# Optimization experiments

Hardware: AMD Instinct MI355X
Metric: run time of the kernel (lower is better)

## Reference

```python
import jax, jax.numpy as jnp
import numpy as np

B, T, C, H = 2, 2048, 1024, 16
D = C // H  # head_dim = 64


def setup_inputs() -> dict:
    key = jax.random.key(0)
    k1, k2, k3 = jax.random.split(key, 3)
    scale = 0.02
    return {
        "x": jax.random.normal(k1, (B, T, C), dtype=jnp.float32),
        "w_qkv": jax.random.normal(k2, (C, 3 * C), dtype=jnp.float32) * scale,
        "b_qkv": jnp.zeros((3 * C,), dtype=jnp.float32),
        "w_out": jax.random.normal(k3, (C, C), dtype=jnp.float32) * scale,
        "b_out": jnp.zeros((C,), dtype=jnp.float32),
    }


def reference(x, w_qkv, b_qkv, w_out, b_out):
    b, t, c = x.shape
    qkv = x @ w_qkv + b_qkv                       # [b, t, 3c]
    q, k, v = jnp.split(qkv, 3, axis=-1)
    # [b, t, c] -> [b, h, t, d]
    q = q.reshape(b, t, H, D).transpose(0, 2, 1, 3)
    k = k.reshape(b, t, H, D).transpose(0, 2, 1, 3)
    v = v.reshape(b, t, H, D).transpose(0, 2, 1, 3)
    scores = jnp.einsum("bhqd,bhkd->bhqk", q, k) / jnp.sqrt(jnp.asarray(D, dtype=q.dtype))
    causal = jnp.tril(jnp.ones((t, t), dtype=bool))
    scores = jnp.where(causal, scores, jnp.finfo(scores.dtype).min)
    attn = jax.nn.softmax(scores, axis=-1)        # [b, h, q, k]
    out = jnp.einsum("bhqk,bhkd->bhqd", attn, v)  # [b, h, t, d]
    out = out.transpose(0, 2, 1, 3).reshape(b, t, c)
    return out @ w_out + b_out
```

## Files before the change

kernel.cpp:

```cpp
#include <hip/hip_runtime.h>

#define B_ 2
#define T_ 2048
#define C_ 1024
#define H_ 16
#define D_ 64

using bf16x8 = __attribute__((ext_vector_type(8))) short;
using f32x4  = __attribute__((ext_vector_type(4))) float;

static __device__ __forceinline__ short f2bf(float f) {
  unsigned u = __builtin_bit_cast(unsigned, f);
  unsigned r = u + 0x7fffu + ((u >> 16) & 1u);
  return (short)(r >> 16);
}

#define GLD16(gp, lp) __builtin_amdgcn_global_load_lds( \
    (const __attribute__((address_space(1))) void*)(gp), \
    (__attribute__((address_space(3))) void*)(lp), 16, 0, 0)

__global__ __launch_bounds__(256) void cast_f32_bf16(const float* __restrict__ in,
                                                     short* __restrict__ out) {
  int i = blockIdx.x * blockDim.x + threadIdx.x;
  float4 v = ((const float4*)in)[i];
  short4 o;
  o.x = f2bf(v.x); o.y = f2bf(v.y); o.z = f2bf(v.z); o.w = f2bf(v.w);
  ((short4*)out)[i] = o;
}

__global__ __launch_bounds__(256) void transpose_cast(const float* __restrict__ in,
                                                      short* __restrict__ out,
                                                      int R, int N) {
  __shared__ float tile[32][33];
  int bx = blockIdx.x * 32, by = blockIdx.y * 32;
  int tx = threadIdx.x, ty = threadIdx.y;
  #pragma unroll
  for (int j = 0; j < 32; j += 8)
    tile[ty + j][tx] = in[(size_t)(by + ty + j) * N + bx + tx];
  __syncthreads();
  #pragma unroll
  for (int j = 0; j < 32; j += 8)
    out[(size_t)(bx + ty + j) * R + by + tx] = f2bf(tile[tx][ty + j]);
}

__global__ __launch_bounds__(256) void gemm_qkv(const short* __restrict__ A,
                                                const short* __restrict__ Bt,
                                                const float* __restrict__ bias,
                                                short* __restrict__ Qo,
                                                short* __restrict__ Ko,
                                                short* __restrict__ Vo) {
  __shared__ short sA[128 * 64];
  __shared__ short sB[128 * 64];
  const int tid = threadIdx.x;
  const int w = tid >> 6, lane = tid & 63;
  const int wm = w >> 1, wn = w & 1;
  const int g = lane >> 4, r16 = lane & 15;
  const int m0 = blockIdx.x * 128, n0 = blockIdx.y * 128;
  const int krow = lane >> 3, kslot = lane & 7;

  f32x4 acc[4][4] = {};

  for (int k0 = 0; k0 < 1024; k0 += 64) {
    __syncthreads();
    #pragma unroll
    for (int p = 0; p < 4; ++p) {
      int rbase = w * 32 + p * 8;
      int row = rbase + krow;
      GLD16(&A[(size_t)(m0 + row) * 1024 + k0 + ((kslot ^ (row & 7)) * 8)], &sA[rbase * 64]);
      GLD16(&Bt[(size_t)(n0 + row) * 1024 + k0 + ((kslot ^ (row & 7)) * 8)], &sB[rbase * 64]);
    }
    __syncthreads();
    bf16x8 af[4][2], bf[4][2];
    #pragma unroll
    for (int mi = 0; mi < 4; ++mi) {
      int row = wm * 64 + mi * 16 + r16;
      #pragma unroll
      for (int c = 0; c < 2; ++c)
        af[mi][c] = *(const bf16x8*)&sA[row * 64 + (((c * 4 + g) ^ (row & 7)) * 8)];
    }
    #pragma unroll
    for (int ni = 0; ni < 4; ++ni) {
      int row = wn * 64 + ni * 16 + r16;
      #pragma unroll
      for (int c = 0; c < 2; ++c)
        bf[ni][c] = *(const bf16x8*)&sB[row * 64 + (((c * 4 + g) ^ (row & 7)) * 8)];
    }
    __builtin_amdgcn_s_setprio(1);
    #pragma unroll
    for (int mi = 0; mi < 4; ++mi)
      #pragma unroll
      for (int ni = 0; ni < 4; ++ni) {
        acc[mi][ni] = __builtin_amdgcn_mfma_f32_16x16x32_bf16(af[mi][0], bf[ni][0], acc[mi][ni], 0, 0, 0);
        acc[mi][ni] = __builtin_amdgcn_mfma_f32_16x16x32_bf16(af[mi][1], bf[ni][1], acc[mi][ni], 0, 0, 0);
      }
    __builtin_amdgcn_s_setprio(0);
  }

  #pragma unroll
  for (int mi = 0; mi < 4; ++mi) {
    #pragma unroll
    for (int ni = 0; ni < 4; ++ni) {
      int n = n0 + wn * 64 + ni * 16 + r16;
      float bv = bias[n];
      int which = n >> 10;
      int c = n & 1023;
      int hh = c >> 6, d = c & 63;
      short* dst = (which == 0) ? Qo : ((which == 1) ? Ko : Vo);
      float sc = (which == 0) ? 0.18033688f : 1.0f;
      #pragma unroll
      for (int rr = 0; rr < 4; ++rr) {
        int m = m0 + wm * 64 + mi * 16 + g * 4 + rr;
        int b = m >> 11, t = m & 2047;
        dst[(size_t)((b * H_ + hh) * T_ + t) * D_ + d] = f2bf((acc[mi][ni][rr] + bv) * sc);
      }
    }
  }
}

__global__ __launch_bounds__(256) void gemm_out(const short* __restrict__ A,
                                                const short* __restrict__ Bt,
                                                const float* __restrict__ bias,
                                                float* __restrict__ Out) {
  __shared__ short sA[128 * 64];
  __shared__ short sB[128 * 64];
  const int tid = threadIdx.x;
  const int w = tid >> 6, lane = tid & 63;
  const int wm = w >> 1, wn = w & 1;
  const int g = lane >> 4, r16 = lane & 15;
  const int m0 = blockIdx.x * 128, n0 = blockIdx.y * 128;
  const int krow = lane >> 3, kslot = lane & 7;

  f32x4 acc[4][4] = {};

  for (int k0 = 0; k0 < 1024; k0 += 64) {
    __syncthreads();
    #pragma unroll
    for (int p = 0; p < 4; ++p) {
      int rbase = w * 32 + p * 8;
      int row = rbase + krow;
      GLD16(&A[(size_t)(m0 + row) * 1024 + k0 + ((kslot ^ (row & 7)) * 8)], &sA[rbase * 64]);
      GLD16(&Bt[(size_t)(n0 + row) * 1024 + k0 + ((kslot ^ (row & 7)) * 8)], &sB[rbase * 64]);
    }
    __syncthreads();
    bf16x8 af[4][2], bf[4][2];
    #pragma unroll
    for (int mi = 0; mi < 4; ++mi) {
      int row = wm * 64 + mi * 16 + r16;
      #pragma unroll
      for (int c = 0; c < 2; ++c)
        af[mi][c] = *(const bf16x8*)&sA[row * 64 + (((c * 4 + g) ^ (row & 7)) * 8)];
    }
    #pragma unroll
    for (int ni = 0; ni < 4; ++ni) {
      int row = wn * 64 + ni * 16 + r16;
      #pragma unroll
      for (int c = 0; c < 2; ++c)
        bf[ni][c] = *(const bf16x8*)&sB[row * 64 + (((c * 4 + g) ^ (row & 7)) * 8)];
    }
    __builtin_amdgcn_s_setprio(1);
    #pragma unroll
    for (int mi = 0; mi < 4; ++mi)
      #pragma unroll
      for (int ni = 0; ni < 4; ++ni) {
        acc[mi][ni] = __builtin_amdgcn_mfma_f32_16x16x32_bf16(af[mi][0], bf[ni][0], acc[mi][ni], 0, 0, 0);
        acc[mi][ni] = __builtin_amdgcn_mfma_f32_16x16x32_bf16(af[mi][1], bf[ni][1], acc[mi][ni], 0, 0, 0);
      }
    __builtin_amdgcn_s_setprio(0);
  }

  #pragma unroll
  for (int mi = 0; mi < 4; ++mi) {
    #pragma unroll
    for (int ni = 0; ni < 4; ++ni) {
      int n = n0 + wn * 64 + ni * 16 + r16;
      float bv = bias[n];
      #pragma unroll
      for (int rr = 0; rr < 4; ++rr) {
        int m = m0 + wm * 64 + mi * 16 + g * 4 + rr;
        Out[(size_t)m * 1024 + n] = acc[mi][ni][rr] + bv;
      }
    }
  }
}

__global__ __launch_bounds__(256, 4) void attn_fwd(const short* __restrict__ Q,
                                                   const short* __restrict__ K,
                                                   const short* __restrict__ V,
                                                   short* __restrict__ O) {
  __shared__ short sK[3][64 * 64];
  __shared__ short vT[2][64 * 64];

  const int tid = threadIdx.x;
  const int w = tid >> 6, lane = tid & 63;
  const int g = lane >> 4, r16 = lane & 15;
  const int bh = blockIdx.x;
  const int b = bh >> 4, hh = bh & 15;
  const int qi = 31 - (int)blockIdx.y;
  const int q0 = qi * 64;

  const short* Qh = Q + (size_t)bh * T_ * D_;
  const short* Kh = K + (size_t)bh * T_ * D_;
  const short* Vh = V + (size_t)bh * T_ * D_;

  const int krow_in_wave = lane >> 3;
  const int kslot = lane & 7;
  const int kp = tid & 31;
  const int vd0 = (tid >> 5) * 8;
  const int vchunk = (kp >> 4) * 4 + ((kp & 7) >> 1);
  const int velem  = ((kp >> 3) & 1) * 4 + 2 * (kp & 1);

  const int qrow_a = q0 + w * 16 + r16;
  bf16x8 qf[2];
  qf[0] = *(const bf16x8*)&Qh[(size_t)qrow_a * 64 + g * 8];
  qf[1] = *(const bf16x8*)&Qh[(size_t)qrow_a * 64 + 32 + g * 8];

  f32x4 o[4] = {};
  float m_ = -1e30f, l_ = 0.f;

  const int nkt = qi + 1;

  {
    int4 v0 = *(const int4*)&Vh[(size_t)(2 * kp) * 64 + vd0];
    int4 v1 = *(const int4*)&Vh[(size_t)(2 * kp + 1) * 64 + vd0];
    #pragma unroll
    for (int p = 0; p < 2; ++p) {
      int row = w * 16 + p * 8 + krow_in_wave;
      GLD16(&Kh[(size_t)row * 64 + ((kslot ^ (row & 7)) * 8)], &sK[0][(w * 16 + p * 8) * 64]);
    }
    if (nkt > 1) {
      #pragma unroll
      for (int p = 0; p < 2; ++p) {
        int row = w * 16 + p * 8 + krow_in_wave;
        GLD16(&Kh[(size_t)(64 + row) * 64 + ((kslot ^ (row & 7)) * 8)],
              &sK[1][(w * 16 + p * 8) * 64]);
      }
    }
    const short* a0 = (const short*)&v0;
    const short* a1 = (const short*)&v1;
    #pragma unroll
    for (int j = 0; j < 8; ++j) {
      int d = vd0 + j;
      int val = ((int)(unsigned short)a0[j]) | (((int)(unsigned short)a1[j]) << 16);
      *(int*)&vT[0][d * 64 + ((vchunk ^ j) * 8) + velem] = val;
    }
    if (nkt > 1) asm volatile("s_waitcnt vmcnt(2)" ::: "memory");
    else         asm volatile("s_waitcnt vmcnt(0)" ::: "memory");
    asm volatile("s_waitcnt lgkmcnt(0)" ::: "memory");
    __builtin_amdgcn_sched_barrier(0);
    __builtin_amdgcn_s_barrier();
    __builtin_amdgcn_sched_barrier(0);
  }

  for (int kt = 0; kt < nkt; ++kt) {
    const int cur3 = kt % 3;
    const int curv = kt & 1;
    const bool pf1 = (kt + 1 < nkt);
    const bool pf2 = (kt + 2 < nkt);

    int4 vn0, vn1;
    if (pf1) {
      const int k1 = (kt + 1) * 64;
      vn0 = *(const int4*)&Vh[(size_t)(k1 + 2 * kp) * 64 + vd0];
      vn1 = *(const int4*)&Vh[(size_t)(k1 + 2 * kp + 1) * 64 + vd0];
    }
    if (pf2) {
      const int k2 = (kt + 2) * 64;
      const int nb = (kt + 2) % 3;
      #pragma unroll
      for (int p = 0; p < 2; ++p) {
        int row = w * 16 + p * 8 + krow_in_wave;
        GLD16(&Kh[(size_t)(k2 + row) * 64 + ((kslot ^ (row & 7)) * 8)],
              &sK[nb][(w * 16 + p * 8) * 64]);
      }
    }
    __builtin_amdgcn_sched_barrier(0);

    f32x4 s[4] = {};
    __builtin_amdgcn_s_setprio(1);
    #pragma unroll
    for (int nt = 0; nt < 4; ++nt) {
      const int row = nt * 16 + r16;
      const int sw8 = r16 & 7;
      bf16x8 kf0 = *(const bf16x8*)&sK[cur3][row * 64 + ((g ^ sw8) * 8)];
      bf16x8 kf1 = *(const bf16x8*)&sK[cur3][row * 64 + (((4 + g) ^ sw8) * 8)];
      s[nt] = __builtin_amdgcn_mfma_f32_16x16x32_bf16(kf0, qf[0], s[nt], 0, 0, 0);
      s[nt] = __builtin_amdgcn_mfma_f32_16x16x32_bf16(kf1, qf[1], s[nt], 0, 0, 0);
    }
    __builtin_amdgcn_s_setprio(0);

    if (kt == nkt - 1) {
      const int qrow = w * 16 + r16;
      #pragma unroll
      for (int nt = 0; nt < 4; ++nt)
        #pragma unroll
        for (int rr = 0; rr < 4; ++rr)
          if (nt * 16 + 4 * g + rr > qrow) s[nt][rr] = -1e30f;
    }
    float pmax = s[0][0];
    #pragma unroll
    for (int nt = 0; nt < 4; ++nt)
      #pragma unroll
      for (int rr = 0; rr < 4; ++rr)
        pmax = fmaxf(pmax, s[nt][rr]);
    pmax = fmaxf(pmax, __shfl_xor(pmax, 16));
    pmax = fmaxf(pmax, __shfl_xor(pmax, 32));
    if (!__all(pmax - m_ <= 8.0f)) {
      float mn = fmaxf(m_, pmax);
      float al = __builtin_amdgcn_exp2f(m_ - mn);
      m_ = mn;
      l_ *= al;
      float av[4];
      #pragma unroll
      for (int rr = 0; rr < 4; ++rr) av[rr] = __shfl(al, 4 * g + rr, 16);
      #pragma unroll
      for (int nt = 0; nt < 4; ++nt)
        #pragma unroll
        for (int rr = 0; rr < 4; ++rr) o[nt][rr] *= av[rr];
    }
    float rs = 0.f;
    #pragma unroll
    for (int nt = 0; nt < 4; ++nt)
      #pragma unroll
      for (int rr = 0; rr < 4; ++rr) {
        float p = __builtin_amdgcn_exp2f(s[nt][rr] - m_);
        s[nt][rr] = p;
        rs += p;
      }
    rs += __shfl_xor(rs, 16);
    rs += __shfl_xor(rs, 32);
    l_ += rs;
    int pk[8];
    #pragma unroll
    for (int nt = 0; nt < 4; ++nt)
      #pragma unroll
      for (int h = 0; h < 2; ++h)
        asm("v_cvt_pk_bf16_f32 %0, %1, %2"
            : "=v"(pk[nt * 2 + h])
            : "v"(s[nt][2 * h]), "v"(s[nt][2 * h + 1]));

    bf16x8 pa[2];
    {
      int4 t0; t0.x = pk[0]; t0.y = pk[1]; t0.z = pk[2]; t0.w = pk[3];
      int4 t1; t1.x = pk[4]; t1.y = pk[5]; t1.z = pk[6]; t1.w = pk[7];
      pa[0] = __builtin_bit_cast(bf16x8, t0);
      pa[1] = __builtin_bit_cast(bf16x8, t1);
    }
    __builtin_amdgcn_s_setprio(1);
    #pragma unroll
    for (int nt = 0; nt < 4; ++nt) {
      const int d = nt * 16 + r16;
      bf16x8 vb0 = *(const bf16x8*)&vT[curv][d * 64 + ((g ^ (d & 7)) * 8)];
      bf16x8 vb1 = *(const bf16x8*)&vT[curv][d * 64 + (((4 + g) ^ (d & 7)) * 8)];
      o[nt] = __builtin_amdgcn_mfma_f32_16x16x32_bf16(pa[0], vb0, o[nt], 0, 0, 0);
      o[nt] = __builtin_amdgcn_mfma_f32_16x16x32_bf16(pa[1], vb1, o[nt], 0, 0, 0);
    }
    __builtin_amdgcn_s_setprio(0);

    if (pf1) {
      const short* a0 = (const short*)&vn0;
      const short* a1 = (const short*)&vn1;
      #pragma unroll
      for (int j = 0; j < 8; ++j) {
        int d = vd0 + j;
        int val = ((int)(unsigned short)a0[j]) | (((int)(unsigned short)a1[j]) << 16);
        *(int*)&vT[curv ^ 1][d * 64 + ((vchunk ^ j) * 8) + velem] = val;
      }
      if (pf2) asm volatile("s_waitcnt vmcnt(2)" ::: "memory");
      else     asm volatile("s_waitcnt vmcnt(0)" ::: "memory");
      asm volatile("s_waitcnt lgkmcnt(0)" ::: "memory");
      __builtin_amdgcn_sched_barrier(0);
      __builtin_amdgcn_s_barrier();
      __builtin_amdgcn_sched_barrier(0);
    }
  }

  float lv[4];
  #pragma unroll
  for (int rr = 0; rr < 4; ++rr) lv[rr] = __shfl(l_, 4 * g + rr, 16);
  #pragma unroll
  for (int nt = 0; nt < 4; ++nt) {
    int d = nt * 16 + r16;
    #pragma unroll
    for (int rr = 0; rr < 4; ++rr) {
      int t = q0 + w * 16 + 4 * g + rr;
      O[(size_t)(b * T_ + t) * C_ + hh * 64 + d] = f2bf(o[nt][rr] / lv[rr]);
    }
  }
}

extern "C" void kernel_launch(void* const* d_in, const int* in_sizes, int n_in,
                              void* d_out, int out_size, void* d_ws, size_t ws_size,
                              hipStream_t stream) {
  const float* x     = (const float*)d_in[0];
  const float* w_qkv = (const float*)d_in[1];
  const float* b_qkv = (const float*)d_in[2];
  const float* w_out = (const float*)d_in[3];
  const float* b_out = (const float*)d_in[4];
  float* out = (float*)d_out;

  char* ws = (char*)d_ws;
  if (ws_size < (size_t)(40u << 20)) return;

  short* xb     = (short*)(ws);
  short* wqkvT  = (short*)(ws + ((size_t)8u << 20));
  short* woutT  = (short*)(ws + ((size_t)14u << 20));
  short* Qb     = (short*)(ws + ((size_t)16u << 20));
  short* Kb     = (short*)(ws + ((size_t)24u << 20));
  short* Vb     = (short*)(ws + ((size_t)32u << 20));
  short* attn_o = xb;

  cast_f32_bf16<<<4096, 256, 0, stream>>>(x, xb);
  transpose_cast<<<dim3(96, 32), dim3(32, 8), 0, stream>>>(w_qkv, wqkvT, 1024, 3072);
  transpose_cast<<<dim3(32, 32), dim3(32, 8), 0, stream>>>(w_out, woutT, 1024, 1024);
  gemm_qkv<<<dim3(32, 24), 256, 0, stream>>>(xb, wqkvT, b_qkv, Qb, Kb, Vb);
  attn_fwd<<<dim3(32, 32), 256, 0, stream>>>(Qb, Kb, Vb, attn_o);
  gemm_out<<<dim3(32, 8), 256, 0, stream>>>(attn_o, woutT, b_out, out);
}
```

Baseline: 125.1 us.

## Write V transposed and permuted from QKV GEMM; attention reads K/V directly to registers

The QKV GEMM epilogue now stores V as a per-head D x T layout with a permuted token order, so the attention kernel can load V fragments straight from global memory in MFMA operand order. The attention kernel drops all LDS staging, barriers and the in-kernel V transpose. Each block now has 2 waves and each wave owns 32 query rows (two 16-row groups), which reuses each K/V fragment twice. Removing LDS and synchronisation costs redundant global loads per wave, since K and V are no longer shared across waves, and the transposed V store in the GEMM epilogue is strided.

```diff
diff --git a/kernel.cpp b/kernel.cpp
--- a/kernel.cpp
+++ b/kernel.cpp
@@ -105,13 +105,19 @@
       int which = n >> 10;
       int c = n & 1023;
       int hh = c >> 6, d = c & 63;
-      short* dst = (which == 0) ? Qo : ((which == 1) ? Ko : Vo);
       float sc = (which == 0) ? 0.18033688f : 1.0f;
       #pragma unroll
       for (int rr = 0; rr < 4; ++rr) {
         int m = m0 + wm * 64 + mi * 16 + g * 4 + rr;
         int b = m >> 11, t = m & 2047;
-        dst[(size_t)((b * H_ + hh) * T_ + t) * D_ + d] = f2bf((acc[mi][ni][rr] + bv) * sc);
+        short val = f2bf((acc[mi][ni][rr] + bv) * sc);
+        if (which == 2) {
+          int tp = (t & ~0x1C) | ((t & 0xC) << 1) | ((t & 0x10) >> 2);
+          Vo[(size_t)((b * H_ + hh) * D_ + d) * T_ + tp] = val;
+        } else {
+          short* dst = (which == 0) ? Qo : Ko;
+          dst[(size_t)((b * H_ + hh) * T_ + t) * D_ + d] = val;
+        }
       }
     }
   }
@@ -183,207 +189,157 @@
   }
 }
 
-__global__ __launch_bounds__(256, 4) void attn_fwd(const short* __restrict__ Q,
+__global__ __launch_bounds__(128, 2) void attn_fwd(const short* __restrict__ Q,
                                                    const short* __restrict__ K,
-                                                   const short* __restrict__ V,
+                                                   const short* __restrict__ Vt,
                                                    short* __restrict__ O) {
-  __shared__ short sK[3][64 * 64];
-  __shared__ short vT[2][64 * 64];
-
   const int tid = threadIdx.x;
   const int w = tid >> 6, lane = tid & 63;
   const int g = lane >> 4, r16 = lane & 15;
   const int bh = blockIdx.x;
   const int b = bh >> 4, hh = bh & 15;
-  const int qi = 31 - (int)blockIdx.y;
-  const int q0 = qi * 64;
+  const int qt = 31 - (int)blockIdx.y;
+  const int qs = qt * 64 + w * 32;
 
   const short* Qh = Q + (size_t)bh * T_ * D_;
   const short* Kh = K + (size_t)bh * T_ * D_;
-  const short* Vh = V + (size_t)bh * T_ * D_;
-
-  const int krow_in_wave = lane >> 3;
-  const int kslot = lane & 7;
-  const int kp = tid & 31;
-  const int vd0 = (tid >> 5) * 8;
-  const int vchunk = (kp >> 4) * 4 + ((kp & 7) >> 1);
-  const int velem  = ((kp >> 3) & 1) * 4 + 2 * (kp & 1);
-
-  const int qrow_a = q0 + w * 16 + r16;
-  bf16x8 qf[2];
-  qf[0] = *(const bf16x8*)&Qh[(size_t)qrow_a * 64 + g * 8];
-  qf[1] = *(const bf16x8*)&Qh[(size_t)qrow_a * 64 + 32 + g * 8];
-
-  f32x4 o[4] = {};
-  float m_ = -1e30f, l_ = 0.f;
-
-  const int nkt = qi + 1;
-
-  {
-    int4 v0 = *(const int4*)&Vh[(size_t)(2 * kp) * 64 + vd0];
-    int4 v1 = *(const int4*)&Vh[(size_t)(2 * kp + 1) * 64 + vd0];
-    #pragma unroll
-    for (int p = 0; p < 2; ++p) {
-      int row = w * 16 + p * 8 + krow_in_wave;
-      GLD16(&Kh[(size_t)row * 64 + ((kslot ^ (row & 7)) * 8)], &sK[0][(w * 16 + p * 8) * 64]);
-    }
-    if (nkt > 1) {
-      #pragma unroll
-      for (int p = 0; p < 2; ++p) {
-        int row = w * 16 + p * 8 + krow_in_wave;
-        GLD16(&Kh[(size_t)(64 + row) * 64 + ((kslot ^ (row & 7)) * 8)],
-              &sK[1][(w * 16 + p * 8) * 64]);
-      }
-    }
-    const short* a0 = (const short*)&v0;
-    const short* a1 = (const short*)&v1;
-    #pragma unroll
-    for (int j = 0; j < 8; ++j) {
-      int d = vd0 + j;
-      int val = ((int)(unsigned short)a0[j]) | (((int)(unsigned short)a1[j]) << 16);
-      *(int*)&vT[0][d * 64 + ((vchunk ^ j) * 8) + velem] = val;
-    }
-    if (nkt > 1) asm volatile("s_waitcnt vmcnt(2)" ::: "memory");
-    else         asm volatile("s_waitcnt vmcnt(0)" ::: "memory");
-    asm volatile("s_waitcnt lgkmcnt(0)" ::: "memory");
-    __builtin_amdgcn_sched_barrier(0);
-    __builtin_amdgcn_s_barrier();
-    __builtin_amdgcn_sched_barrier(0);
+  const short* Vh = Vt + (size_t)bh * D_ * T_;
+
+  bf16x8 qf[2][2];
+  #pragma unroll
+  for (int u = 0; u < 2; ++u) {
+    const size_t qoff = (size_t)(qs + u * 16 + r16) * 64;
+    qf[u][0] = *(const bf16x8*)&Qh[qoff + g * 8];
+    qf[u][1] = *(const bf16x8*)&Qh[qoff + 32 + g * 8];
+  }
+
+  f32x4 o[2][4] = {};
+  float m_[2] = {-1e30f, -1e30f}, l_[2] = {0.f, 0.f};
+
+  const int nkt = qs / 64 + 1;
+
+  bf16x8 kf[4][2];
+  #pragma unroll
+  for (int nt = 0; nt < 4; ++nt) {
+    const size_t koff = (size_t)(nt * 16 + r16) * 64;
+    kf[nt][0] = *(const bf16x8*)&Kh[koff + g * 8];
+    kf[nt][1] = *(const bf16x8*)&Kh[koff + 32 + g * 8];
   }
 
   for (int kt = 0; kt < nkt; ++kt) {
-    const int cur3 = kt % 3;
-    const int curv = kt & 1;
-    const bool pf1 = (kt + 1 < nkt);
-    const bool pf2 = (kt + 2 < nkt);
-
-    int4 vn0, vn1;
-    if (pf1) {
-      const int k1 = (kt + 1) * 64;
-      vn0 = *(const int4*)&Vh[(size_t)(k1 + 2 * kp) * 64 + vd0];
-      vn1 = *(const int4*)&Vh[(size_t)(k1 + 2 * kp + 1) * 64 + vd0];
-    }
-    if (pf2) {
-      const int k2 = (kt + 2) * 64;
-      const int nb = (kt + 2) % 3;
-      #pragma unroll
-      for (int p = 0; p < 2; ++p) {
-        int row = w * 16 + p * 8 + krow_in_wave;
-        GLD16(&Kh[(size_t)(k2 + row) * 64 + ((kslot ^ (row & 7)) * 8)],
-              &sK[nb][(w * 16 + p * 8) * 64]);
-      }
-    }
-    __builtin_amdgcn_sched_barrier(0);
-
-    f32x4 s[4] = {};
+    const int k0 = kt * 64;
+
+    bf16x8 vb[4][2];
+    #pragma unroll
+    for (int nt = 0; nt < 4; ++nt) {
+      const size_t voff = (size_t)(nt * 16 + r16) * T_ + k0;
+      vb[nt][0] = *(const bf16x8*)&Vh[voff + g * 8];
+      vb[nt][1] = *(const bf16x8*)&Vh[voff + 32 + g * 8];
+    }
+
+    f32x4 s[2][4] = {};
     __builtin_amdgcn_s_setprio(1);
     #pragma unroll
     for (int nt = 0; nt < 4; ++nt) {
-      const int row = nt * 16 + r16;
-      const int sw8 = r16 & 7;
-      bf16x8 kf0 = *(const bf16x8*)&sK[cur3][row * 64 + ((g ^ sw8) * 8)];
-      bf16x8 kf1 = *(const bf16x8*)&sK[cur3][row * 64 + (((4 + g) ^ sw8) * 8)];
-      s[nt] = __builtin_amdgcn_mfma_f32_16x16x32_bf16(kf0, qf[0], s[nt], 0, 0, 0);
-      s[nt] = __builtin_amdgcn_mfma_f32_16x16x32_bf16(kf1, qf[1], s[nt], 0, 0, 0);
+      s[0][nt] = __builtin_amdgcn_mfma_f32_16x16x32_bf16(kf[nt][0], qf[0][0], s[0][nt], 0, 0, 0);
+      s[0][nt] = __builtin_amdgcn_mfma_f32_16x16x32_bf16(kf[nt][1], qf[0][1], s[0][nt], 0, 0, 0);
+      s[1][nt] = __builtin_amdgcn_mfma_f32_16x16x32_bf16(kf[nt][0], qf[1][0], s[1][nt], 0, 0, 0);
+      s[1][nt] = __builtin_amdgcn_mfma_f32_16x16x32_bf16(kf[nt][1], qf[1][1], s[1][nt], 0, 0, 0);
     }
     __builtin_amdgcn_s_setprio(0);
 
-    if (kt == nkt - 1) {
-      const int qrow = w * 16 + r16;
+    if (kt + 1 < nkt) {
+      const int k1 = k0 + 64;
+      #pragma unroll
+      for (int nt = 0; nt < 4; ++nt) {
+        const size_t koff = (size_t)(k1 + nt * 16 + r16) * 64;
+        kf[nt][0] = *(const bf16x8*)&Kh[koff + g * 8];
+        kf[nt][1] = *(const bf16x8*)&Kh[koff + 32 + g * 8];
+      }
+    }
+
+    bf16x8 pa[2][2];
+    #pragma unroll
+    for (int u = 0; u < 2; ++u) {
+      if (kt == nkt - 1) {
+        const int qrow = qs + u * 16 + r16;
+        #pragma unroll
+        for (int nt = 0; nt < 4; ++nt)
+          #pragma unroll
+          for (int rr = 0; rr < 4; ++rr)
+            if (k0 + nt * 16 + 4 * g + rr > qrow) s[u][nt][rr] = -1e30f;
+      }
+      float pmax = s[u][0][0];
       #pragma unroll
       for (int nt = 0; nt < 4; ++nt)
         #pragma unroll
         for (int rr = 0; rr < 4; ++rr)
-          if (nt * 16 + 4 * g + rr > qrow) s[nt][rr] = -1e30f;
-    }
-    float pmax = s[0][0];
-    #pragma unroll
-    for (int nt = 0; nt < 4; ++nt)
-      #pragma unroll
-      for (int rr = 0; rr < 4; ++rr)
-        pmax = fmaxf(pmax, s[nt][rr]);
-    pmax = fmaxf(pmax, __shfl_xor(pmax, 16));
-    pmax = fmaxf(pmax, __shfl_xor(pmax, 32));
-    if (!__all(pmax - m_ <= 8.0f)) {
-      float mn = fmaxf(m_, pmax);
-      float al = __builtin_amdgcn_exp2f(m_ - mn);
-      m_ = mn;
-      l_ *= al;
-      float av[4];
-      #pragma unroll
-      for (int rr = 0; rr < 4; ++rr) av[rr] = __shfl(al, 4 * g + rr, 16);
+          pmax = fmaxf(pmax, s[u][nt][rr]);
+      pmax = fmaxf(pmax, __shfl_xor(pmax, 16));
+      pmax = fmaxf(pmax, __shfl_xor(pmax, 32));
+      if (!__all(pmax - m_[u] <= 8.0f)) {
+        float mn = fmaxf(m_[u], pmax);
+        float al = __builtin_amdgcn_exp2f(m_[u] - mn);
+        m_[u] = mn;
+        l_[u] *= al;
+        float av[4];
+        #pragma unroll
+        for (int rr = 0; rr < 4; ++rr) av[rr] = __shfl(al, 4 * g + rr, 16);
+        #pragma unroll
+        for (int nt = 0; nt < 4; ++nt)
+          #pragma unroll
+          for (int rr = 0; rr < 4; ++rr) o[u][nt][rr] *= av[rr];
+      }
+      float rs = 0.f;
       #pragma unroll
       for (int nt = 0; nt < 4; ++nt)
         #pragma unroll
-        for (int rr = 0; rr < 4; ++rr) o[nt][rr] *= av[rr];
-    }
-    float rs = 0.f;
-    #pragma unroll
-    for (int nt = 0; nt < 4; ++nt)
-      #pragma unroll
-      for (int rr = 0; rr < 4; ++rr) {
-        float p = __builtin_amdgcn_exp2f(s[nt][rr] - m_);
-        s[nt][rr] = p;
-        rs += p;
-      }
-    rs += __shfl_xor(rs, 16);
-    rs += __shfl_xor(rs, 32);
-    l_ += rs;
-    int pk[8];
-    #pragma unroll
-    for (int nt = 0; nt < 4; ++nt)
-      #pragma unroll
-      for (int h = 0; h < 2; ++h)
-        asm("v_cvt_pk_bf16_f32 %0, %1, %2"
-            : "=v"(pk[nt * 2 + h])
-            : "v"(s[nt][2 * h]), "v"(s[nt][2 * h + 1]));
-
-    bf16x8 pa[2];
-    {
+        for (int rr = 0; rr < 4; ++rr) {
+          float p = __builtin_amdgcn_exp2f(s[u][nt][rr] - m_[u]);
+          s[u][nt][rr] = p;
+          rs += p;
+        }
+      rs += __shfl_xor(rs, 16);
+      rs += __shfl_xor(rs, 32);
+      l_[u] += rs;
+      int pk[8];
+      #pragma unroll
+      for (int nt = 0; nt < 4; ++nt)
+        #pragma unroll
+        for (int h = 0; h < 2; ++h)
+          asm("v_cvt_pk_bf16_f32 %0, %1, %2"
+              : "=v"(pk[nt * 2 + h])
+              : "v"(s[u][nt][2 * h]), "v"(s[u][nt][2 * h + 1]));
       int4 t0; t0.x = pk[0]; t0.y = pk[1]; t0.z = pk[2]; t0.w = pk[3];
       int4 t1; t1.x = pk[4]; t1.y = pk[5]; t1.z = pk[6]; t1.w = pk[7];
-      pa[0] = __builtin_bit_cast(bf16x8, t0);
-      pa[1] = __builtin_bit_cast(bf16x8, t1);
-    }
+      pa[u][0] = __builtin_bit_cast(bf16x8, t0);
+      pa[u][1] = __builtin_bit_cast(bf16x8, t1);
+    }
+
     __builtin_amdgcn_s_setprio(1);
     #pragma unroll
     for (int nt = 0; nt < 4; ++nt) {
-      const int d = nt * 16 + r16;
-      bf16x8 vb0 = *(const bf16x8*)&vT[curv][d * 64 + ((g ^ (d & 7)) * 8)];
-      bf16x8 vb1 = *(const bf16x8*)&vT[curv][d * 64 + (((4 + g) ^ (d & 7)) * 8)];
-      o[nt] = __builtin_amdgcn_mfma_f32_16x16x32_bf16(pa[0], vb0, o[nt], 0, 0, 0);
-      o[nt] = __builtin_amdgcn_mfma_f32_16x16x32_bf16(pa[1], vb1, o[nt], 0, 0, 0);
+      o[0][nt] = __builtin_amdgcn_mfma_f32_16x16x32_bf16(pa[0][0], vb[nt][0], o[0][nt], 0, 0, 0);
+      o[0][nt] = __builtin_amdgcn_mfma_f32_16x16x32_bf16(pa[0][1], vb[nt][1], o[0][nt], 0, 0, 0);
+      o[1][nt] = __builtin_amdgcn_mfma_f32_16x16x32_bf16(pa[1][0], vb[nt][0], o[1][nt], 0, 0, 0);
+      o[1][nt] = __builtin_amdgcn_mfma_f32_16x16x32_bf16(pa[1][1], vb[nt][1], o[1][nt], 0, 0, 0);
     }
     __builtin_amdgcn_s_setprio(0);
-
-    if (pf1) {
-      const short* a0 = (const short*)&vn0;
-      const short* a1 = (const short*)&vn1;
-      #pragma unroll
-      for (int j = 0; j < 8; ++j) {
-        int d = vd0 + j;
-        int val = ((int)(unsigned short)a0[j]) | (((int)(unsigned short)a1[j]) << 16);
-        *(int*)&vT[curv ^ 1][d * 64 + ((vchunk ^ j) * 8) + velem] = val;
-      }
-      if (pf2) asm volatile("s_waitcnt vmcnt(2)" ::: "memory");
-      else     asm volatile("s_waitcnt vmcnt(0)" ::: "memory");
-      asm volatile("s_waitcnt lgkmcnt(0)" ::: "memory");
-      __builtin_amdgcn_sched_barrier(0);
-      __builtin_amdgcn_s_barrier();
-      __builtin_amdgcn_sched_barrier(0);
-    }
-  }
-
-  float lv[4];
-  #pragma unroll
-  for (int rr = 0; rr < 4; ++rr) lv[rr] = __shfl(l_, 4 * g + rr, 16);
-  #pragma unroll
-  for (int nt = 0; nt < 4; ++nt) {
-    int d = nt * 16 + r16;
-    #pragma unroll
-    for (int rr = 0; rr < 4; ++rr) {
-      int t = q0 + w * 16 + 4 * g + rr;
-      O[(size_t)(b * T_ + t) * C_ + hh * 64 + d] = f2bf(o[nt][rr] / lv[rr]);
+  }
+
+  #pragma unroll
+  for (int u = 0; u < 2; ++u) {
+    float lv[4];
+    #pragma unroll
+    for (int rr = 0; rr < 4; ++rr) lv[rr] = __shfl(l_[u], 4 * g + rr, 16);
+    #pragma unroll
+    for (int nt = 0; nt < 4; ++nt) {
+      int d = nt * 16 + r16;
+      #pragma unroll
+      for (int rr = 0; rr < 4; ++rr) {
+        int t = qs + u * 16 + 4 * g + rr;
+        O[(size_t)(b * T_ + t) * C_ + hh * 64 + d] = f2bf(o[u][nt][rr] / lv[rr]);
+      }
     }
   }
 }
@@ -406,13 +362,13 @@
   short* woutT  = (short*)(ws + ((size_t)14u << 20));
   short* Qb     = (short*)(ws + ((size_t)16u << 20));
   short* Kb     = (short*)(ws + ((size_t)24u << 20));
-  short* Vb     = (short*)(ws + ((size_t)32u << 20));
+  short* Vtb    = (short*)(ws + ((size_t)32u << 20));
   short* attn_o = xb;
 
   cast_f32_bf16<<<4096, 256, 0, stream>>>(x, xb);
   transpose_cast<<<dim3(96, 32), dim3(32, 8), 0, stream>>>(w_qkv, wqkvT, 1024, 3072);
   transpose_cast<<<dim3(32, 32), dim3(32, 8), 0, stream>>>(w_out, woutT, 1024, 1024);
-  gemm_qkv<<<dim3(32, 24), 256, 0, stream>>>(xb, wqkvT, b_qkv, Qb, Kb, Vb);
-  attn_fwd<<<dim3(32, 32), 256, 0, stream>>>(Qb, Kb, Vb, attn_o);
+  gemm_qkv<<<dim3(32, 24), 256, 0, stream>>>(xb, wqkvT, b_qkv, Qb, Kb, Vtb);
+  attn_fwd<<<dim3(32, 32), 128, 0, stream>>>(Qb, Kb, Vtb, attn_o);
   gemm_out<<<dim3(32, 8), 256, 0, stream>>>(attn_o, woutT, b_out, out);
 }
```

New measurement: 156.1 us. 24.8% more time.

## Write V transposed from QKV GEMM and load V fragments directly in attention

Applied to the files above, without the earlier changes.

The QKV GEMM epilogue now stages V tiles through shared memory and writes V in [head, d, t] layout. The attention kernel then loads V MFMA operands straight from global memory into registers, so it no longer transposes V into LDS each tile. K prefetch drops from triple to double buffering, and the hand-tuned waitcnt/barrier sequence becomes a plain __syncthreads per iteration. This removes LDS transpose work and LDS footprint, but V loads now hit global/L2 on the critical path without prefetch, and the extra sync may reduce overlap.

```diff
diff --git a/kernel.cpp b/kernel.cpp
--- a/kernel.cpp
+++ b/kernel.cpp
@@ -48,9 +48,10 @@
                                                 const float* __restrict__ bias,
                                                 short* __restrict__ Qo,
                                                 short* __restrict__ Ko,
-                                                short* __restrict__ Vo) {
-  __shared__ short sA[128 * 64];
-  __shared__ short sB[128 * 64];
+                                                short* __restrict__ Vt) {
+  __shared__ short smem[128 * 132];
+  short* sA = smem;
+  short* sB = smem + 128 * 64;
   const int tid = threadIdx.x;
   const int w = tid >> 6, lane = tid & 63;
   const int wm = w >> 1, wn = w & 1;
@@ -96,23 +97,52 @@
     __builtin_amdgcn_s_setprio(0);
   }
 
-  #pragma unroll
-  for (int mi = 0; mi < 4; ++mi) {
-    #pragma unroll
-    for (int ni = 0; ni < 4; ++ni) {
-      int n = n0 + wn * 64 + ni * 16 + r16;
-      float bv = bias[n];
-      int which = n >> 10;
-      int c = n & 1023;
-      int hh = c >> 6, d = c & 63;
-      short* dst = (which == 0) ? Qo : ((which == 1) ? Ko : Vo);
-      float sc = (which == 0) ? 0.18033688f : 1.0f;
-      #pragma unroll
-      for (int rr = 0; rr < 4; ++rr) {
-        int m = m0 + wm * 64 + mi * 16 + g * 4 + rr;
-        int b = m >> 11, t = m & 2047;
-        dst[(size_t)((b * H_ + hh) * T_ + t) * D_ + d] = f2bf((acc[mi][ni][rr] + bv) * sc);
-      }
+  if (n0 < 2048) {
+    const int which = n0 >> 10;
+    short* dst = (which == 0) ? Qo : Ko;
+    const float sc = (which == 0) ? 0.18033688f : 1.0f;
+    #pragma unroll
+    for (int mi = 0; mi < 4; ++mi) {
+      #pragma unroll
+      for (int ni = 0; ni < 4; ++ni) {
+        int n = n0 + wn * 64 + ni * 16 + r16;
+        float bv = bias[n];
+        int c = n & 1023;
+        int hh = c >> 6, d = c & 63;
+        #pragma unroll
+        for (int rr = 0; rr < 4; ++rr) {
+          int m = m0 + wm * 64 + mi * 16 + g * 4 + rr;
+          int b = m >> 11, t = m & 2047;
+          dst[(size_t)((b * H_ + hh) * T_ + t) * D_ + d] = f2bf((acc[mi][ni][rr] + bv) * sc);
+        }
+      }
+    }
+  } else {
+    __syncthreads();
+    #pragma unroll
+    for (int mi = 0; mi < 4; ++mi) {
+      #pragma unroll
+      for (int ni = 0; ni < 4; ++ni) {
+        int nn = wn * 64 + ni * 16 + r16;
+        float bv = bias[n0 + nn];
+        #pragma unroll
+        for (int rr = 0; rr < 4; ++rr) {
+          int tm = wm * 64 + mi * 16 + g * 4 + rr;
+          smem[tm * 132 + nn] = f2bf(acc[mi][ni][rr] + bv);
+        }
+      }
+    }
+    __syncthreads();
+    const int tinv = (lane & ~0x1C) | ((lane & 0x18) >> 1) | ((lane & 4) << 2);
+    const int b2 = m0 >> 11, t0l = m0 & 2047;
+    const int head0 = b2 * H_ + ((n0 - 2048) >> 6);
+    #pragma unroll 8
+    for (int i = 0; i < 64; ++i) {
+      int half = i >> 5, nnl = i & 31;
+      int nn = w * 32 + nnl;
+      int d = nn & 63, hh2 = nn >> 6;
+      short val = smem[(half * 64 + tinv) * 132 + nn];
+      Vt[((size_t)(head0 + hh2) * D_ + d) * T_ + t0l + half * 64 + lane] = val;
     }
   }
 }
@@ -185,10 +215,9 @@
 
 __global__ __launch_bounds__(256, 4) void attn_fwd(const short* __restrict__ Q,
                                                    const short* __restrict__ K,
-                                                   const short* __restrict__ V,
+                                                   const short* __restrict__ Vt,
                                                    short* __restrict__ O) {
-  __shared__ short sK[3][64 * 64];
-  __shared__ short vT[2][64 * 64];
+  __shared__ short sK[2][64 * 64];
 
   const int tid = threadIdx.x;
   const int w = tid >> 6, lane = tid & 63;
@@ -200,14 +229,10 @@
 
   const short* Qh = Q + (size_t)bh * T_ * D_;
   const short* Kh = K + (size_t)bh * T_ * D_;
-  const short* Vh = V + (size_t)bh * T_ * D_;
+  const short* Vh = Vt + (size_t)bh * D_ * T_;
 
   const int krow_in_wave = lane >> 3;
   const int kslot = lane & 7;
-  const int kp = tid & 31;
-  const int vd0 = (tid >> 5) * 8;
-  const int vchunk = (kp >> 4) * 4 + ((kp & 7) >> 1);
-  const int velem  = ((kp >> 3) & 1) * 4 + 2 * (kp & 1);
 
   const int qrow_a = q0 + w * 16 + r16;
   bf16x8 qf[2];
@@ -219,61 +244,33 @@
 
   const int nkt = qi + 1;
 
-  {
-    int4 v0 = *(const int4*)&Vh[(size_t)(2 * kp) * 64 + vd0];
-    int4 v1 = *(const int4*)&Vh[(size_t)(2 * kp + 1) * 64 + vd0];
-    #pragma unroll
-    for (int p = 0; p < 2; ++p) {
-      int row = w * 16 + p * 8 + krow_in_wave;
-      GLD16(&Kh[(size_t)row * 64 + ((kslot ^ (row & 7)) * 8)], &sK[0][(w * 16 + p * 8) * 64]);
-    }
-    if (nkt > 1) {
+  #pragma unroll
+  for (int p = 0; p < 2; ++p) {
+    int row = w * 16 + p * 8 + krow_in_wave;
+    GLD16(&Kh[(size_t)row * 64 + ((kslot ^ (row & 7)) * 8)], &sK[0][(w * 16 + p * 8) * 64]);
+  }
+  __syncthreads();
+
+  for (int kt = 0; kt < nkt; ++kt) {
+    const int cur = kt & 1;
+    const int k0 = kt * 64;
+
+    bf16x8 vb[4][2];
+    #pragma unroll
+    for (int nt = 0; nt < 4; ++nt) {
+      const size_t voff = (size_t)(nt * 16 + r16) * T_ + k0;
+      vb[nt][0] = *(const bf16x8*)&Vh[voff + g * 8];
+      vb[nt][1] = *(const bf16x8*)&Vh[voff + 32 + g * 8];
+    }
+    if (kt + 1 < nkt) {
+      const int k1 = k0 + 64;
       #pragma unroll
       for (int p = 0; p < 2; ++p) {
         int row = w * 16 + p * 8 + krow_in_wave;
-        GLD16(&Kh[(size_t)(64 + row) * 64 + ((kslot ^ (row & 7)) * 8)],
-              &sK[1][(w * 16 + p * 8) * 64]);
-      }
-    }
-    const short* a0 = (const short*)&v0;
-    const short* a1 = (const short*)&v1;
-    #pragma unroll
-    for (int j = 0; j < 8; ++j) {
-      int d = vd0 + j;
-      int val = ((int)(unsigned short)a0[j]) | (((int)(unsigned short)a1[j]) << 16);
-      *(int*)&vT[0][d * 64 + ((vchunk ^ j) * 8) + velem] = val;
-    }
-    if (nkt > 1) asm volatile("s_waitcnt vmcnt(2)" ::: "memory");
-    else         asm volatile("s_waitcnt vmcnt(0)" ::: "memory");
-    asm volatile("s_waitcnt lgkmcnt(0)" ::: "memory");
-    __builtin_amdgcn_sched_barrier(0);
-    __builtin_amdgcn_s_barrier();
-    __builtin_amdgcn_sched_barrier(0);
-  }
-
-  for (int kt = 0; kt < nkt; ++kt) {
-    const int cur3 = kt % 3;
-    const int curv = kt & 1;
-    const bool pf1 = (kt + 1 < nkt);
-    const bool pf2 = (kt + 2 < nkt);
-
-    int4 vn0, vn1;
-    if (pf1) {
-      const int k1 = (kt + 1) * 64;
-      vn0 = *(const int4*)&Vh[(size_t)(k1 + 2 * kp) * 64 + vd0];
-      vn1 = *(const int4*)&Vh[(size_t)(k1 + 2 * kp + 1) * 64 + vd0];
-    }
-    if (pf2) {
-      const int k2 = (kt + 2) * 64;
-      const int nb = (kt + 2) % 3;
-      #pragma unroll
-      for (int p = 0; p < 2; ++p) {
-        int row = w * 16 + p * 8 + krow_in_wave;
-        GLD16(&Kh[(size_t)(k2 + row) * 64 + ((kslot ^ (row & 7)) * 8)],
-              &sK[nb][(w * 16 + p * 8) * 64]);
-      }
-    }
-    __builtin_amdgcn_sched_barrier(0);
+        GLD16(&Kh[(size_t)(k1 + row) * 64 + ((kslot ^ (row & 7)) * 8)],
+              &sK[cur ^ 1][(w * 16 + p * 8) * 64]);
+      }
+    }
 
     f32x4 s[4] = {};
     __builtin_amdgcn_s_setprio(1);
@@ -281,8 +278,8 @@
     for (int nt = 0; nt < 4; ++nt) {
       const int row = nt * 16 + r16;
       const int sw8 = r16 & 7;
-      bf16x8 kf0 = *(const bf16x8*)&sK[cur3][row * 64 + ((g ^ sw8) * 8)];
-      bf16x8 kf1 = *(const bf16x8*)&sK[cur3][row * 64 + (((4 + g) ^ sw8) * 8)];
+      bf16x8 kf0 = *(const bf16x8*)&sK[cur][row * 64 + ((g ^ sw8) * 8)];
+      bf16x8 kf1 = *(const bf16x8*)&sK[cur][row * 64 + (((4 + g) ^ sw8) * 8)];
       s[nt] = __builtin_amdgcn_mfma_f32_16x16x32_bf16(kf0, qf[0], s[nt], 0, 0, 0);
       s[nt] = __builtin_amdgcn_mfma_f32_16x16x32_bf16(kf1, qf[1], s[nt], 0, 0, 0);
     }
@@ -348,30 +345,12 @@
     __builtin_amdgcn_s_setprio(1);
     #pragma unroll
     for (int nt = 0; nt < 4; ++nt) {
-      const int d = nt * 16 + r16;
-      bf16x8 vb0 = *(const bf16x8*)&vT[curv][d * 64 + ((g ^ (d & 7)) * 8)];
-      bf16x8 vb1 = *(const bf16x8*)&vT[curv][d * 64 + (((4 + g) ^ (d & 7)) * 8)];
-      o[nt] = __builtin_amdgcn_mfma_f32_16x16x32_bf16(pa[0], vb0, o[nt], 0, 0, 0);
-      o[nt] = __builtin_amdgcn_mfma_f32_16x16x32_bf16(pa[1], vb1, o[nt], 0, 0, 0);
+      o[nt] = __builtin_amdgcn_mfma_f32_16x16x32_bf16(pa[0], vb[nt][0], o[nt], 0, 0, 0);
+      o[nt] = __builtin_amdgcn_mfma_f32_16x16x32_bf16(pa[1], vb[nt][1], o[nt], 0, 0, 0);
     }
     __builtin_amdgcn_s_setprio(0);
 
-    if (pf1) {
-      const short* a0 = (const short*)&vn0;
-      const short* a1 = (const short*)&vn1;
-      #pragma unroll
-      for (int j = 0; j < 8; ++j) {
-        int d = vd0 + j;
-        int val = ((int)(unsigned short)a0[j]) | (((int)(unsigned short)a1[j]) << 16);
-        *(int*)&vT[curv ^ 1][d * 64 + ((vchunk ^ j) * 8) + velem] = val;
-      }
-      if (pf2) asm volatile("s_waitcnt vmcnt(2)" ::: "memory");
-      else     asm volatile("s_waitcnt vmcnt(0)" ::: "memory");
-      asm volatile("s_waitcnt lgkmcnt(0)" ::: "memory");
-      __builtin_amdgcn_sched_barrier(0);
-      __builtin_amdgcn_s_barrier();
-      __builtin_amdgcn_sched_barrier(0);
-    }
+    __syncthreads();
   }
 
   float lv[4];
@@ -406,13 +385,13 @@
   short* woutT  = (short*)(ws + ((size_t)14u << 20));
   short* Qb     = (short*)(ws + ((size_t)16u << 20));
   short* Kb     = (short*)(ws + ((size_t)24u << 20));
-  short* Vb     = (short*)(ws + ((size_t)32u << 20));
+  short* Vtb    = (short*)(ws + ((size_t)32u << 20));
   short* attn_o = xb;
 
   cast_f32_bf16<<<4096, 256, 0, stream>>>(x, xb);
   transpose_cast<<<dim3(96, 32), dim3(32, 8), 0, stream>>>(w_qkv, wqkvT, 1024, 3072);
   transpose_cast<<<dim3(32, 32), dim3(32, 8), 0, stream>>>(w_out, woutT, 1024, 1024);
-  gemm_qkv<<<dim3(32, 24), 256, 0, stream>>>(xb, wqkvT, b_qkv, Qb, Kb, Vb);
-  attn_fwd<<<dim3(32, 32), 256, 0, stream>>>(Qb, Kb, Vb, attn_o);
+  gemm_qkv<<<dim3(32, 24), 256, 0, stream>>>(xb, wqkvT, b_qkv, Qb, Kb, Vtb);
+  attn_fwd<<<dim3(32, 32), 256, 0, stream>>>(Qb, Kb, Vtb, attn_o);
   gemm_out<<<dim3(32, 8), 256, 0, stream>>>(attn_o, woutT, b_out, out);
 }
```

New measurement: 159.8 us. 1.28x slower.

## Switch K to double buffering and defer softmax row-sum reduction to epilogue

Applied to the files above, without the earlier changes.

Replaces the three-stage K ring (two tiles ahead, hand-tuned vmcnt waits) with a two-stage K/V double buffer using plain __syncthreads. Moves the cross-lane row-max reduction inside the rare rescale branch. Keeps per-lane partial row sums, reducing them only once after the loop, which removes shuffles from every iteration. In exchange, K prefetch distance drops to one tile and the generic barrier may wait on all outstanding loads, exposing more memory latency.

```diff
diff --git a/kernel.cpp b/kernel.cpp
--- a/kernel.cpp
+++ b/kernel.cpp
@@ -187,7 +187,7 @@
                                                    const short* __restrict__ K,
                                                    const short* __restrict__ V,
                                                    short* __restrict__ O) {
-  __shared__ short sK[3][64 * 64];
+  __shared__ short sK[2][64 * 64];
   __shared__ short vT[2][64 * 64];
 
   const int tid = threadIdx.x;
@@ -219,22 +219,14 @@
 
   const int nkt = qi + 1;
 
+  #pragma unroll
+  for (int p = 0; p < 2; ++p) {
+    int row = w * 16 + p * 8 + krow_in_wave;
+    GLD16(&Kh[(size_t)row * 64 + ((kslot ^ (row & 7)) * 8)], &sK[0][(w * 16 + p * 8) * 64]);
+  }
   {
     int4 v0 = *(const int4*)&Vh[(size_t)(2 * kp) * 64 + vd0];
     int4 v1 = *(const int4*)&Vh[(size_t)(2 * kp + 1) * 64 + vd0];
-    #pragma unroll
-    for (int p = 0; p < 2; ++p) {
-      int row = w * 16 + p * 8 + krow_in_wave;
-      GLD16(&Kh[(size_t)row * 64 + ((kslot ^ (row & 7)) * 8)], &sK[0][(w * 16 + p * 8) * 64]);
-    }
-    if (nkt > 1) {
-      #pragma unroll
-      for (int p = 0; p < 2; ++p) {
-        int row = w * 16 + p * 8 + krow_in_wave;
-        GLD16(&Kh[(size_t)(64 + row) * 64 + ((kslot ^ (row & 7)) * 8)],
-              &sK[1][(w * 16 + p * 8) * 64]);
-      }
-    }
     const short* a0 = (const short*)&v0;
     const short* a1 = (const short*)&v1;
     #pragma unroll
@@ -243,37 +235,26 @@
       int val = ((int)(unsigned short)a0[j]) | (((int)(unsigned short)a1[j]) << 16);
       *(int*)&vT[0][d * 64 + ((vchunk ^ j) * 8) + velem] = val;
     }
-    if (nkt > 1) asm volatile("s_waitcnt vmcnt(2)" ::: "memory");
-    else         asm volatile("s_waitcnt vmcnt(0)" ::: "memory");
-    asm volatile("s_waitcnt lgkmcnt(0)" ::: "memory");
-    __builtin_amdgcn_sched_barrier(0);
-    __builtin_amdgcn_s_barrier();
-    __builtin_amdgcn_sched_barrier(0);
-  }
+  }
+  __syncthreads();
 
   for (int kt = 0; kt < nkt; ++kt) {
-    const int cur3 = kt % 3;
-    const int curv = kt & 1;
-    const bool pf1 = (kt + 1 < nkt);
-    const bool pf2 = (kt + 2 < nkt);
+    const int cur = kt & 1, nxt = cur ^ 1;
+    const int k0 = kt * 64;
+    const bool pf = (kt + 1 < nkt);
 
     int4 vn0, vn1;
-    if (pf1) {
-      const int k1 = (kt + 1) * 64;
+    if (pf) {
+      const int k1 = k0 + 64;
+      #pragma unroll
+      for (int p = 0; p < 2; ++p) {
+        int row = w * 16 + p * 8 + krow_in_wave;
+        GLD16(&Kh[(size_t)(k1 + row) * 64 + ((kslot ^ (row & 7)) * 8)],
+              &sK[nxt][(w * 16 + p * 8) * 64]);
+      }
       vn0 = *(const int4*)&Vh[(size_t)(k1 + 2 * kp) * 64 + vd0];
       vn1 = *(const int4*)&Vh[(size_t)(k1 + 2 * kp + 1) * 64 + vd0];
     }
-    if (pf2) {
-      const int k2 = (kt + 2) * 64;
-      const int nb = (kt + 2) % 3;
-      #pragma unroll
-      for (int p = 0; p < 2; ++p) {
-        int row = w * 16 + p * 8 + krow_in_wave;
-        GLD16(&Kh[(size_t)(k2 + row) * 64 + ((kslot ^ (row & 7)) * 8)],
-              &sK[nb][(w * 16 + p * 8) * 64]);
-      }
-    }
-    __builtin_amdgcn_sched_barrier(0);
 
     f32x4 s[4] = {};
     __builtin_amdgcn_s_setprio(1);
@@ -281,8 +262,8 @@
     for (int nt = 0; nt < 4; ++nt) {
       const int row = nt * 16 + r16;
       const int sw8 = r16 & 7;
-      bf16x8 kf0 = *(const bf16x8*)&sK[cur3][row * 64 + ((g ^ sw8) * 8)];
-      bf16x8 kf1 = *(const bf16x8*)&sK[cur3][row * 64 + (((4 + g) ^ sw8) * 8)];
+      bf16x8 kf0 = *(const bf16x8*)&sK[cur][row * 64 + ((g ^ sw8) * 8)];
+      bf16x8 kf1 = *(const bf16x8*)&sK[cur][row * 64 + (((4 + g) ^ sw8) * 8)];
       s[nt] = __builtin_amdgcn_mfma_f32_16x16x32_bf16(kf0, qf[0], s[nt], 0, 0, 0);
       s[nt] = __builtin_amdgcn_mfma_f32_16x16x32_bf16(kf1, qf[1], s[nt], 0, 0, 0);
     }
@@ -302,10 +283,10 @@
       #pragma unroll
       for (int rr = 0; rr < 4; ++rr)
         pmax = fmaxf(pmax, s[nt][rr]);
-    pmax = fmaxf(pmax, __shfl_xor(pmax, 16));
-    pmax = fmaxf(pmax, __shfl_xor(pmax, 32));
     if (!__all(pmax - m_ <= 8.0f)) {
-      float mn = fmaxf(m_, pmax);
+      float rmax = fmaxf(pmax, __shfl_xor(pmax, 16));
+      rmax = fmaxf(rmax, __shfl_xor(rmax, 32));
+      float mn = fmaxf(m_, rmax);
       float al = __builtin_amdgcn_exp2f(m_ - mn);
       m_ = mn;
       l_ *= al;
@@ -326,8 +307,6 @@
         s[nt][rr] = p;
         rs += p;
       }
-    rs += __shfl_xor(rs, 16);
-    rs += __shfl_xor(rs, 32);
     l_ += rs;
     int pk[8];
     #pragma unroll
@@ -349,34 +328,31 @@
     #pragma unroll
     for (int nt = 0; nt < 4; ++nt) {
       const int d = nt * 16 + r16;
-      bf16x8 vb0 = *(const bf16x8*)&vT[curv][d * 64 + ((g ^ (d & 7)) * 8)];
-      bf16x8 vb1 = *(const bf16x8*)&vT[curv][d * 64 + (((4 + g) ^ (d & 7)) * 8)];
+      bf16x8 vb0 = *(const bf16x8*)&vT[cur][d * 64 + ((g ^ (d & 7)) * 8)];
+      bf16x8 vb1 = *(const bf16x8*)&vT[cur][d * 64 + (((4 + g) ^ (d & 7)) * 8)];
       o[nt] = __builtin_amdgcn_mfma_f32_16x16x32_bf16(pa[0], vb0, o[nt], 0, 0, 0);
       o[nt] = __builtin_amdgcn_mfma_f32_16x16x32_bf16(pa[1], vb1, o[nt], 0, 0, 0);
     }
     __builtin_amdgcn_s_setprio(0);
 
-    if (pf1) {
+    if (pf) {
       const short* a0 = (const short*)&vn0;
       const short* a1 = (const short*)&vn1;
       #pragma unroll
       for (int j = 0; j < 8; ++j) {
         int d = vd0 + j;
         int val = ((int)(unsigned short)a0[j]) | (((int)(unsigned short)a1[j]) << 16);
-        *(int*)&vT[curv ^ 1][d * 64 + ((vchunk ^ j) * 8) + velem] = val;
-      }
-      if (pf2) asm volatile("s_waitcnt vmcnt(2)" ::: "memory");
-      else     asm volatile("s_waitcnt vmcnt(0)" ::: "memory");
-      asm volatile("s_waitcnt lgkmcnt(0)" ::: "memory");
-      __builtin_amdgcn_sched_barrier(0);
-      __builtin_amdgcn_s_barrier();
-      __builtin_amdgcn_sched_barrier(0);
-    }
-  }
-
+        *(int*)&vT[nxt][d * 64 + ((vchunk ^ j) * 8) + velem] = val;
+      }
+    }
+    __syncthreads();
+  }
+
+  float lt = l_ + __shfl_xor(l_, 16);
+  lt += __shfl_xor(lt, 32);
   float lv[4];
   #pragma unroll
-  for (int rr = 0; rr < 4; ++rr) lv[rr] = __shfl(l_, 4 * g + rr, 16);
+  for (int rr = 0; rr < 4; ++rr) lv[rr] = __shfl(lt, 4 * g + rr, 16);
   #pragma unroll
   for (int nt = 0; nt < 4; ++nt) {
     int d = nt * 16 + r16;
```

Result: faster. 119.3 us (-4.6%).
